# Kernel tuning notes

Measured on AMD Instinct MI355X. Metric: run time of the kernel, lower is better.

The kernel has to match this reference:

```python
import jax, jax.numpy as jnp
import numpy as np

DIM = 1024
NUM_HEADS = 16
HEAD_DIM = DIM // NUM_HEADS
THETA = 10000.0


def apply_rope(x):
    # x: [B, S, H, D]; Llama-style interleaved rotary pairs.
    S, D = x.shape[1], x.shape[3]
    half = D // 2
    inv_freq = THETA ** (-jnp.arange(half, dtype=jnp.float32) * 2.0 / D)  # [D/2]
    angles = jnp.arange(S, dtype=jnp.float32)[:, None] * inv_freq[None, :]  # [S, D/2]
    cos = jnp.cos(angles)[None, :, None, :]  # [1,S,1,D/2]
    sin = jnp.sin(angles)[None, :, None, :]
    x_even = x[..., 0::2]
    x_odd = x[..., 1::2]
    out_even = x_even * cos - x_odd * sin
    out_odd = x_even * sin + x_odd * cos
    out = jnp.stack([out_even, out_odd], axis=-1).reshape(x.shape)
    return out.astype(x.dtype)


def setup_inputs() -> dict:
    key = jax.random.key(0)
    ks = jax.random.split(key, 5)
    B, S = 2, 2048
    x = jax.random.normal(ks[0], (B, S, DIM), dtype=jnp.float32)
    scale = 1.0 / np.sqrt(DIM)
    Wq = jax.random.normal(ks[1], (DIM, DIM), dtype=jnp.float32) * scale
    Wk = jax.random.normal(ks[2], (DIM, DIM), dtype=jnp.float32) * scale
    Wv = jax.random.normal(ks[3], (DIM, DIM), dtype=jnp.float32) * scale
    Wo = jax.random.normal(ks[4], (DIM, DIM), dtype=jnp.float32) * scale
    return {"x": x, "Wq": Wq, "Wk": Wk, "Wv": Wv, "Wo": Wo}


def reference(x, Wq, Wk, Wv, Wo):
    B, S, _ = x.shape
    # torch Linear: y = x @ W^T
    q = (x @ Wq.T).reshape(B, S, NUM_HEADS, HEAD_DIM)
    k = (x @ Wk.T).reshape(B, S, NUM_HEADS, HEAD_DIM)
    v = (x @ Wv.T).reshape(B, S, NUM_HEADS, HEAD_DIM)
    q = apply_rope(q)
    k = apply_rope(k)
    # causal SDPA, scale = 1/sqrt(head_dim)
    scale = 1.0 / np.sqrt(HEAD_DIM).astype(np.float32)
    scores = jnp.einsum("bqhd,bkhd->bhqk", q, k) * scale  # [B,H,S,S]
    causal = jnp.tril(jnp.ones((S, S), dtype=bool))
    scores = jnp.where(causal[None, None], scores, jnp.finfo(scores.dtype).min)
    attn = jax.nn.softmax(scores, axis=-1)
    y = jnp.einsum("bhqk,bkhd->bqhd", attn, v).reshape(B, S, DIM)
    return y @ Wo.T
```

## Files before the change

kernel.cpp:

```cpp
#include <hip/hip_runtime.h>
#include <hip/hip_bf16.h>

typedef __attribute__((ext_vector_type(8))) __bf16 bf16x8;
typedef __attribute__((ext_vector_type(4))) __bf16 bf16x4;
typedef __attribute__((ext_vector_type(4))) float f32x4;
typedef __attribute__((ext_vector_type(16))) float f32x16;
typedef __attribute__((ext_vector_type(2))) unsigned int uint2v;
typedef __attribute__((ext_vector_type(4))) unsigned int uint4v;

#define DIM 1024
#define SLEN 2048
#define NH 16
#define HD 64

__device__ __forceinline__ f32x4 MFMA(bf16x8 a, bf16x8 b, f32x4 c) {
    return __builtin_amdgcn_mfma_f32_16x16x32_bf16(a, b, c, 0, 0, 0);
}
__device__ __forceinline__ f32x16 MFMA32(bf16x8 a, bf16x8 b, f32x16 c) {
    return __builtin_amdgcn_mfma_f32_32x32x16_bf16(a, b, c, 0, 0, 0);
}
__device__ __forceinline__ unsigned cvtpk(float a, float b) {
    unsigned r;
    asm("v_cvt_pk_bf16_f32 %0, %1, %2" : "=v"(r) : "v"(a), "v"(b));
    return r;
}

__global__ __launch_bounds__(256) void cvt_bf16(const float* __restrict__ in,
                                                __bf16* __restrict__ out, int n) {
    int i = (blockIdx.x * blockDim.x + threadIdx.x) * 8;
    if (i >= n) return;
    f32x4 a = *reinterpret_cast<const f32x4*>(in + i);
    f32x4 b = *reinterpret_cast<const f32x4*>(in + i + 4);
    bf16x8 o;
#pragma unroll
    for (int j = 0; j < 4; ++j) { o[j] = (__bf16)a[j]; o[j + 4] = (__bf16)b[j]; }
    *reinterpret_cast<bf16x8*>(out + i) = o;
}

__global__ __launch_bounds__(256) void cvt_w4(const float* __restrict__ w0,
                                              const float* __restrict__ w1,
                                              const float* __restrict__ w2,
                                              const float* __restrict__ w3,
                                              __bf16* __restrict__ o0,
                                              __bf16* __restrict__ o1,
                                              __bf16* __restrict__ o2,
                                              __bf16* __restrict__ o3) {
    int s = blockIdx.y;
    const float* in = s == 0 ? w0 : s == 1 ? w1 : s == 2 ? w2 : w3;
    __bf16* out = s == 0 ? o0 : s == 1 ? o1 : s == 2 ? o2 : o3;
    int i = (blockIdx.x * blockDim.x + threadIdx.x) * 8;
    f32x4 a = *reinterpret_cast<const f32x4*>(in + i);
    f32x4 b = *reinterpret_cast<const f32x4*>(in + i + 4);
    bf16x8 o;
#pragma unroll
    for (int j = 0; j < 4; ++j) { o[j] = (__bf16)a[j]; o[j + 4] = (__bf16)b[j]; }
    *reinterpret_cast<bf16x8*>(out + i) = o;
}

__global__ __launch_bounds__(256) void rope2(__bf16* __restrict__ q,
                                             __bf16* __restrict__ k) {
    __bf16* t = blockIdx.y == 0 ? q : k;
    const float scale = blockIdx.y == 0 ? 0.18033688011112042f : 1.0f;
    int idx = blockIdx.x * blockDim.x + threadIdx.x;
    int row = idx >> 9;
    int p = idx & 511;
    int head = p >> 5;
    int j = p & 31;
    int s = row & (SLEN - 1);
    float inv = expf(-0.28782313662425574f * (float)j);
    float angle = (float)s * inv;
    float sn, cs;
    sincosf(angle, &sn, &cs);
    size_t base = (size_t)row * DIM + head * HD + 2 * j;
    float e = (float)t[base], o = (float)t[base + 1];
    t[base] = (__bf16)((e * cs - o * sn) * scale);
    t[base + 1] = (__bf16)((e * sn + o * cs) * scale);
}

__global__ __launch_bounds__(256) void gemm_qkv(const __bf16* __restrict__ X,
                                                const __bf16* __restrict__ Wq,
                                                const __bf16* __restrict__ Wk,
                                                const __bf16* __restrict__ Wv,
                                                __bf16* __restrict__ Qo,
                                                __bf16* __restrict__ Ko,
                                                __bf16* __restrict__ Vt) {
    __shared__ alignas(16) __bf16 Alds[128 * 64];
    __shared__ alignas(16) __bf16 Blds[128 * 64];
    const int tid = threadIdx.x;
    const int lane = tid & 63;
    const int w = tid >> 6;
    const int wr = w >> 1, wc = w & 1;
    const int l15 = lane & 15, lhi = lane >> 4;
    const int l7 = l15 & 7;
    const int m0 = blockIdx.y * 128;
    const int n0g = blockIdx.x * 128;
    const int seg = n0g >> 10;
    const int n0 = n0g & 1023;
    const __bf16* __restrict__ B = seg == 0 ? Wq : seg == 1 ? Wk : Wv;
    const int K = 1024, N = 1024;

    const int lrow = lane >> 3;
    const int scol = ((lane & 7) ^ lrow) * 8;

    f32x4 acc[4][4] = {};

    for (int kt = 0; kt < K; kt += 64) {
#pragma unroll
        for (int c = 0; c < 4; ++c) {
            int r0 = c * 32 + w * 8;
            const __bf16* sa = &X[(size_t)(m0 + r0 + lrow) * K + kt + scol];
            const __bf16* sb = &B[(size_t)(n0 + r0 + lrow) * K + kt + scol];
            __builtin_amdgcn_global_load_lds((const __attribute__((address_space(1))) void*)sa,
                                             (__attribute__((address_space(3))) void*)&Alds[r0 * 64],
                                             16, 0, 0);
            __builtin_amdgcn_global_load_lds((const __attribute__((address_space(1))) void*)sb,
                                             (__attribute__((address_space(3))) void*)&Blds[r0 * 64],
                                             16, 0, 0);
        }
        __syncthreads();
#pragma unroll
        for (int kk = 0; kk < 2; ++kk) {
            bf16x8 af[4], bfr[4];
#pragma unroll
            for (int i = 0; i < 4; ++i) {
                af[i] = *(const bf16x8*)&Alds[(wr * 64 + i * 16 + l15) * 64 + 8 * ((kk * 4 + lhi) ^ l7)];
                bfr[i] = *(const bf16x8*)&Blds[(wc * 64 + i * 16 + l15) * 64 + 8 * ((kk * 4 + lhi) ^ l7)];
            }
            __builtin_amdgcn_s_setprio(1);
#pragma unroll
            for (int i = 0; i < 4; ++i)
#pragma unroll
                for (int j = 0; j < 4; ++j)
                    acc[i][j] = MFMA(af[i], bfr[j], acc[i][j]);
            __builtin_amdgcn_s_setprio(0);
        }
        __syncthreads();
    }
    if (seg < 2) {
        __bf16* __restrict__ O = seg == 0 ? Qo : Ko;
#pragma unroll
        for (int i = 0; i < 4; ++i)
#pragma unroll
            for (int j = 0; j < 4; ++j)
#pragma unroll
                for (int r = 0; r < 4; ++r) {
                    int row = m0 + wr * 64 + i * 16 + lhi * 4 + r;
                    int col = n0 + wc * 64 + j * 16 + l15;
                    O[(size_t)row * N + col] = (__bf16)acc[i][j][r];
                }
    } else {
#pragma unroll
        for (int i = 0; i < 4; ++i)
#pragma unroll
            for (int j = 0; j < 4; ++j) {
                int row = m0 + wr * 64 + i * 16 + lhi * 4;
                int col = n0 + wc * 64 + j * 16 + l15;
                int bb = row >> 11, s = row & 2047;
                int hh = col >> 6, d = col & 63;
                bf16x4 pk;
#pragma unroll
                for (int r = 0; r < 4; ++r) pk[r] = (__bf16)acc[i][j][r];
                *(bf16x4*)&Vt[((size_t)(bb * 16 + hh) * 64 + d) * SLEN + s] = pk;
            }
    }
}

__global__ __launch_bounds__(256) void gemm_o(const __bf16* __restrict__ A,
                                              const __bf16* __restrict__ B,
                                              float* __restrict__ C) {
    __shared__ alignas(16) __bf16 Alds[64 * 64];
    __shared__ alignas(16) __bf16 Blds[128 * 64];
    const int tid = threadIdx.x;
    const int lane = tid & 63;
    const int w = tid >> 6;
    const int wr = w >> 1, wc = w & 1;
    const int l15 = lane & 15, lhi = lane >> 4;
    const int l7 = l15 & 7;
    const int m0 = blockIdx.y * 64;
    const int n0 = blockIdx.x * 128;
    const int K = 1024, N = 1024;

    const int lrow = lane >> 3;
    const int scol = ((lane & 7) ^ lrow) * 8;

    f32x4 acc[2][4] = {};

    for (int kt = 0; kt < K; kt += 64) {
#pragma unroll
        for (int c = 0; c < 2; ++c) {
            int r0 = c * 32 + w * 8;
            const __bf16* sa = &A[(size_t)(m0 + r0 + lrow) * K + kt + scol];
            __builtin_amdgcn_global_load_lds((const __attribute__((address_space(1))) void*)sa,
                                             (__attribute__((address_space(3))) void*)&Alds[r0 * 64],
                                             16, 0, 0);
        }
#pragma unroll
        for (int c = 0; c < 4; ++c) {
            int r0 = c * 32 + w * 8;
            const __bf16* sb = &B[(size_t)(n0 + r0 + lrow) * K + kt + scol];
            __builtin_amdgcn_global_load_lds((const __attribute__((address_space(1))) void*)sb,
                                             (__attribute__((address_space(3))) void*)&Blds[r0 * 64],
                                             16, 0, 0);
        }
        __syncthreads();
#pragma unroll
        for (int kk = 0; kk < 2; ++kk) {
            bf16x8 af[2], bfr[4];
#pragma unroll
            for (int i = 0; i < 2; ++i)
                af[i] = *(const bf16x8*)&Alds[(wr * 32 + i * 16 + l15) * 64 + 8 * ((kk * 4 + lhi) ^ l7)];
#pragma unroll
            for (int j = 0; j < 4; ++j)
                bfr[j] = *(const bf16x8*)&Blds[(wc * 64 + j * 16 + l15) * 64 + 8 * ((kk * 4 + lhi) ^ l7)];
            __builtin_amdgcn_s_setprio(1);
#pragma unroll
            for (int i = 0; i < 2; ++i)
#pragma unroll
                for (int j = 0; j < 4; ++j)
                    acc[i][j] = MFMA(af[i], bfr[j], acc[i][j]);
            __builtin_amdgcn_s_setprio(0);
        }
        __syncthreads();
    }
#pragma unroll
    for (int i = 0; i < 2; ++i)
#pragma unroll
        for (int j = 0; j < 4; ++j)
#pragma unroll
            for (int r = 0; r < 4; ++r) {
                int row = m0 + wr * 32 + i * 16 + lhi * 4 + r;
                int col = n0 + wc * 64 + j * 16 + l15;
                C[(size_t)row * N + col] = acc[i][j][r];
            }
}

__global__ __launch_bounds__(256, 4) void attn_kernel(const __bf16* __restrict__ Q,
                                                      const __bf16* __restrict__ K,
                                                      const __bf16* __restrict__ Vt,
                                                      __bf16* __restrict__ Y) {
    __shared__ __bf16 Klds[2][64 * 64];
    __shared__ __bf16 Vlds[2][64 * 64];

    const int tid = threadIdx.x;
    const int lane = tid & 63;
    const int w = tid >> 6;
    const int qhalf = w & 1, khalf = w >> 1;
    const int l31 = lane & 31;
    const int hi32 = lane >> 5;
    const int l7 = l31 & 7;

    const int id = blockIdx.x;
    const int x = id & 7, jj = id >> 3;
    const int qi = jj >> 2;
    const int g = qi >> 3, r = qi & 7;
    const int qt = g == 0 ? 31 - r : g == 1 ? r : g == 2 ? 23 - r : 8 + r;
    const int bh = 4 * x + (jj & 3);
    const int b = bh >> 4, h = bh & 15;

    const int srow = lane >> 3;
    const int scs = (lane & 7) ^ srow;
    const __bf16* skP = K + (size_t)b * SLEN * DIM + h * HD + (size_t)(8 * w + srow) * DIM + scs * 8;
    const __bf16* svP = Vt + (size_t)bh * 64 * SLEN + (size_t)(8 * w + srow) * SLEN + scs * 8;
    const int dA = (8 * w + srow) * 64;

    auto stage = [&](int buf) {
#pragma unroll
        for (int i = 0; i < 2; ++i) {
            __builtin_amdgcn_global_load_lds(
                (const __attribute__((address_space(1))) void*)(skP + (size_t)i * 32 * DIM),
                (__attribute__((address_space(3))) void*)&Klds[buf][dA + i * 32 * 64], 16, 0, 0);
            __builtin_amdgcn_global_load_lds(
                (const __attribute__((address_space(1))) void*)(svP + (size_t)i * 32 * SLEN),
                (__attribute__((address_space(3))) void*)&Vlds[buf][dA + i * 32 * 64], 16, 0, 0);
        }
        skP += 64 * DIM;
        svP += 64;
    };

    const int qloc = qhalf * 32 + l31;
    const int qg = qt * 64 + qloc;
    const size_t qbase = (size_t)(b * SLEN + qg) * DIM + h * HD;
    bf16x8 qf0 = *(const bf16x8*)&Q[qbase + 0 + 8 * hi32];
    bf16x8 qf1 = *(const bf16x8*)&Q[qbase + 16 + 8 * hi32];
    bf16x8 qf2 = *(const bf16x8*)&Q[qbase + 32 + 8 * hi32];
    bf16x8 qf3 = *(const bf16x8*)&Q[qbase + 48 + 8 * hi32];

    const int krowbase = (khalf * 32 + l31) * 64;
    const int koff0 = krowbase + 8 * ((0 + hi32) ^ l7);
    const int koff1 = krowbase + 8 * ((2 + hi32) ^ l7);
    const int koff2 = krowbase + 8 * ((4 + hi32) ^ l7);
    const int koff3 = krowbase + 8 * ((6 + hi32) ^ l7);
    const int vrow0 = l31 * 64, vrow1 = (32 + l31) * 64;
    const int voff00 = vrow0 + 8 * ((4 * khalf + 0 + hi32) ^ l7);
    const int voff01 = vrow0 + 8 * ((4 * khalf + 2 + hi32) ^ l7);
    const int voff10 = vrow1 + 8 * ((4 * khalf + 0 + hi32) ^ l7);
    const int voff11 = vrow1 + 8 * ((4 * khalf + 2 + hi32) ^ l7);

    bf16x8 ones;
#pragma unroll
    for (int t = 0; t < 8; ++t) ones[t] = (__bf16)1.0f;

    f32x16 acc0 = {}, acc1 = {};
    f32x16 accL = {};

    const int nkt = qt + 1;
    stage(0);
    for (int kt = 0; kt < nkt; ++kt) {
        const int cur = kt & 1;
        __syncthreads();
        if (kt + 1 < nkt) stage(cur ^ 1);
        const __bf16* Kc = Klds[cur];
        const __bf16* Vc = Vlds[cur];

        f32x16 S = {};
        __builtin_amdgcn_s_setprio(1);
        S = MFMA32(*(const bf16x8*)&Kc[koff0], qf0, S);
        S = MFMA32(*(const bf16x8*)&Kc[koff1], qf1, S);
        S = MFMA32(*(const bf16x8*)&Kc[koff2], qf2, S);
        S = MFMA32(*(const bf16x8*)&Kc[koff3], qf3, S);
        __builtin_amdgcn_s_setprio(0);

        if (kt == qt) {
#pragma unroll
            for (int r2 = 0; r2 < 16; ++r2) {
                const int krow = (r2 & 3) + 8 * (r2 >> 2) + 4 * hi32 + 32 * khalf;
                if (krow > qloc) S[r2] = -1e30f;
            }
        }
        float p[16];
#pragma unroll
        for (int r2 = 0; r2 < 16; ++r2) p[r2] = exp2f(S[r2] - 16.0f);

        bf16x8 pf[2];
#pragma unroll
        for (int ss = 0; ss < 2; ++ss) {
            unsigned P01 = cvtpk(p[8 * ss + 0], p[8 * ss + 1]);
            unsigned P23 = cvtpk(p[8 * ss + 2], p[8 * ss + 3]);
            unsigned Q01 = cvtpk(p[8 * ss + 4], p[8 * ss + 5]);
            unsigned Q23 = cvtpk(p[8 * ss + 6], p[8 * ss + 7]);
            uint2v sa = __builtin_amdgcn_permlane32_swap(P01, Q01, false, false);
            uint2v sb = __builtin_amdgcn_permlane32_swap(P23, Q23, false, false);
            uint4v pwv = {sa[0], sb[0], sa[1], sb[1]};
            pf[ss] = __builtin_bit_cast(bf16x8, pwv);
        }

        __builtin_amdgcn_s_setprio(1);
        accL = MFMA32(ones, pf[0], accL);
        accL = MFMA32(ones, pf[1], accL);
        acc0 = MFMA32(*(const bf16x8*)&Vc[voff00], pf[0], acc0);
        acc0 = MFMA32(*(const bf16x8*)&Vc[voff01], pf[1], acc0);
        acc1 = MFMA32(*(const bf16x8*)&Vc[voff10], pf[0], acc1);
        acc1 = MFMA32(*(const bf16x8*)&Vc[voff11], pf[1], acc1);
        __builtin_amdgcn_s_setprio(0);
    }

    float lsum = accL[0];
    float* fbuf = (float*)&Klds[0][0];
    float* lbuf = (float*)&Vlds[0][0];
    __syncthreads();
    if (khalf == 1) {
#pragma unroll
        for (int r2 = 0; r2 < 16; ++r2) {
            fbuf[(qhalf * 2 + 0) * 1024 + r2 * 64 + lane] = acc0[r2];
            fbuf[(qhalf * 2 + 1) * 1024 + r2 * 64 + lane] = acc1[r2];
        }
        lbuf[qhalf * 64 + lane] = lsum;
    }
    __syncthreads();
    if (khalf == 0) {
#pragma unroll
        for (int r2 = 0; r2 < 16; ++r2) {
            acc0[r2] += fbuf[(qhalf * 2 + 0) * 1024 + r2 * 64 + lane];
            acc1[r2] += fbuf[(qhalf * 2 + 1) * 1024 + r2 * 64 + lane];
        }
        lsum += lbuf[qhalf * 64 + lane];
        const float inv = 1.0f / lsum;
        const size_t obase = (size_t)(b * SLEN + qg) * DIM + h * HD;
#pragma unroll
        for (int gg = 0; gg < 4; ++gg) {
            bf16x4 o0, o1;
#pragma unroll
            for (int e = 0; e < 4; ++e) {
                o0[e] = (__bf16)(acc0[gg * 4 + e] * inv);
                o1[e] = (__bf16)(acc1[gg * 4 + e] * inv);
            }
            *(bf16x4*)&Y[obase + 8 * gg + 4 * hi32] = o0;
            *(bf16x4*)&Y[obase + 32 + 8 * gg + 4 * hi32] = o1;
        }
    }
}

extern "C" void kernel_launch(void* const* d_in, const int* in_sizes, int n_in,
                              void* d_out, int out_size, void* d_ws, size_t ws_size,
                              hipStream_t stream) {
    const float* x = (const float*)d_in[0];
    const float* Wq = (const float*)d_in[1];
    const float* Wk = (const float*)d_in[2];
    const float* Wv = (const float*)d_in[3];
    const float* Wo = (const float*)d_in[4];
    float* out = (float*)d_out;

    const size_t XN = (size_t)4096 * 1024;
    const size_t WN = (size_t)1024 * 1024;

    __bf16* xb = (__bf16*)d_ws;
    __bf16* qb = xb + XN;
    __bf16* kb = qb + XN;
    __bf16* vtb = kb + XN;
    __bf16* wqb = vtb + XN;
    __bf16* wkb = wqb + WN;
    __bf16* wvb = wkb + WN;
    __bf16* wob = wvb + WN;
    __bf16* yb = xb;

    cvt_bf16<<<XN / 8 / 256, 256, 0, stream>>>(x, xb, (int)XN);
    dim3 gw(WN / 8 / 256, 4);
    cvt_w4<<<gw, 256, 0, stream>>>(Wq, Wk, Wv, Wo, wqb, wkb, wvb, wob);

    dim3 gq(24, 32);
    gemm_qkv<<<gq, 256, 0, stream>>>(xb, wqb, wkb, wvb, qb, kb, vtb);

    int pairs = 4096 * (DIM / 2);
    dim3 gr(pairs / 256, 2);
    rope2<<<gr, 256, 0, stream>>>(qb, kb);

    attn_kernel<<<1024, 256, 0, stream>>>(qb, kb, vtb, yb);

    dim3 go(8, 64);
    gemm_o<<<go, 256, 0, stream>>>(yb, wob, out);
}
```

Baseline: 109.3 us.

## Load K/V tiles directly from global into registers, dropping LDS staging

The attention kernel no longer stages K and V tiles into double-buffered shared memory via global_load_lds with per-iteration barriers. Each wave now loads its own K and V fragments straight from global memory into registers inside the loop, and shared memory is kept only for the final cross-wave reduction. This removes the per-tile __syncthreads and LDS traffic, but loses explicit prefetch overlap. Each K/V element is also now fetched by two waves, relying on cache hits.

```diff
diff --git a/kernel.cpp b/kernel.cpp
--- a/kernel.cpp
+++ b/kernel.cpp
@@ -238,8 +238,8 @@
                                                       const __bf16* __restrict__ K,
                                                       const __bf16* __restrict__ Vt,
                                                       __bf16* __restrict__ Y) {
-    __shared__ __bf16 Klds[2][64 * 64];
-    __shared__ __bf16 Vlds[2][64 * 64];
+    __shared__ float fbuf[4096];
+    __shared__ float lbuf[128];
 
     const int tid = threadIdx.x;
     const int lane = tid & 63;
@@ -247,7 +247,6 @@
     const int qhalf = w & 1, khalf = w >> 1;
     const int l31 = lane & 31;
     const int hi32 = lane >> 5;
-    const int l7 = l31 & 7;
 
     const int id = blockIdx.x;
     const int x = id & 7, jj = id >> 3;
@@ -257,25 +256,9 @@
     const int bh = 4 * x + (jj & 3);
     const int b = bh >> 4, h = bh & 15;
 
-    const int srow = lane >> 3;
-    const int scs = (lane & 7) ^ srow;
-    const __bf16* skP = K + (size_t)b * SLEN * DIM + h * HD + (size_t)(8 * w + srow) * DIM + scs * 8;
-    const __bf16* svP = Vt + (size_t)bh * 64 * SLEN + (size_t)(8 * w + srow) * SLEN + scs * 8;
-    const int dA = (8 * w + srow) * 64;
-
-    auto stage = [&](int buf) {
-#pragma unroll
-        for (int i = 0; i < 2; ++i) {
-            __builtin_amdgcn_global_load_lds(
-                (const __attribute__((address_space(1))) void*)(skP + (size_t)i * 32 * DIM),
-                (__attribute__((address_space(3))) void*)&Klds[buf][dA + i * 32 * 64], 16, 0, 0);
-            __builtin_amdgcn_global_load_lds(
-                (const __attribute__((address_space(1))) void*)(svP + (size_t)i * 32 * SLEN),
-                (__attribute__((address_space(3))) void*)&Vlds[buf][dA + i * 32 * 64], 16, 0, 0);
-        }
-        skP += 64 * DIM;
-        svP += 64;
-    };
+    const __bf16* kPtr = K + (size_t)(b * SLEN + khalf * 32 + l31) * DIM + h * HD + 8 * hi32;
+    const __bf16* vPtr0 = Vt + (size_t)(bh * 64 + l31) * SLEN + 32 * khalf + 8 * hi32;
+    const __bf16* vPtr1 = vPtr0 + (size_t)32 * SLEN;
 
     const int qloc = qhalf * 32 + l31;
     const int qg = qt * 64 + qloc;
@@ -285,17 +268,6 @@
     bf16x8 qf2 = *(const bf16x8*)&Q[qbase + 32 + 8 * hi32];
     bf16x8 qf3 = *(const bf16x8*)&Q[qbase + 48 + 8 * hi32];
 
-    const int krowbase = (khalf * 32 + l31) * 64;
-    const int koff0 = krowbase + 8 * ((0 + hi32) ^ l7);
-    const int koff1 = krowbase + 8 * ((2 + hi32) ^ l7);
-    const int koff2 = krowbase + 8 * ((4 + hi32) ^ l7);
-    const int koff3 = krowbase + 8 * ((6 + hi32) ^ l7);
-    const int vrow0 = l31 * 64, vrow1 = (32 + l31) * 64;
-    const int voff00 = vrow0 + 8 * ((4 * khalf + 0 + hi32) ^ l7);
-    const int voff01 = vrow0 + 8 * ((4 * khalf + 2 + hi32) ^ l7);
-    const int voff10 = vrow1 + 8 * ((4 * khalf + 0 + hi32) ^ l7);
-    const int voff11 = vrow1 + 8 * ((4 * khalf + 2 + hi32) ^ l7);
-
     bf16x8 ones;
 #pragma unroll
     for (int t = 0; t < 8; ++t) ones[t] = (__bf16)1.0f;
@@ -304,21 +276,27 @@
     f32x16 accL = {};
 
     const int nkt = qt + 1;
-    stage(0);
     for (int kt = 0; kt < nkt; ++kt) {
-        const int cur = kt & 1;
-        __syncthreads();
-        if (kt + 1 < nkt) stage(cur ^ 1);
-        const __bf16* Kc = Klds[cur];
-        const __bf16* Vc = Vlds[cur];
+        bf16x8 k0 = *(const bf16x8*)(kPtr + 0);
+        bf16x8 k1 = *(const bf16x8*)(kPtr + 16);
+        bf16x8 k2 = *(const bf16x8*)(kPtr + 32);
+        bf16x8 k3 = *(const bf16x8*)(kPtr + 48);
+        kPtr += (size_t)64 * DIM;
 
         f32x16 S = {};
         __builtin_amdgcn_s_setprio(1);
-        S = MFMA32(*(const bf16x8*)&Kc[koff0], qf0, S);
-        S = MFMA32(*(const bf16x8*)&Kc[koff1], qf1, S);
-        S = MFMA32(*(const bf16x8*)&Kc[koff2], qf2, S);
-        S = MFMA32(*(const bf16x8*)&Kc[koff3], qf3, S);
+        S = MFMA32(k0, qf0, S);
+        S = MFMA32(k1, qf1, S);
+        S = MFMA32(k2, qf2, S);
+        S = MFMA32(k3, qf3, S);
         __builtin_amdgcn_s_setprio(0);
+
+        bf16x8 v00 = *(const bf16x8*)(vPtr0 + 0);
+        bf16x8 v01 = *(const bf16x8*)(vPtr0 + 16);
+        bf16x8 v10 = *(const bf16x8*)(vPtr1 + 0);
+        bf16x8 v11 = *(const bf16x8*)(vPtr1 + 16);
+        vPtr0 += 64;
+        vPtr1 += 64;
 
         if (kt == qt) {
 #pragma unroll
@@ -347,17 +325,14 @@
         __builtin_amdgcn_s_setprio(1);
         accL = MFMA32(ones, pf[0], accL);
         accL = MFMA32(ones, pf[1], accL);
-        acc0 = MFMA32(*(const bf16x8*)&Vc[voff00], pf[0], acc0);
-        acc0 = MFMA32(*(const bf16x8*)&Vc[voff01], pf[1], acc0);
-        acc1 = MFMA32(*(const bf16x8*)&Vc[voff10], pf[0], acc1);
-        acc1 = MFMA32(*(const bf16x8*)&Vc[voff11], pf[1], acc1);
+        acc0 = MFMA32(v00, pf[0], acc0);
+        acc0 = MFMA32(v01, pf[1], acc0);
+        acc1 = MFMA32(v10, pf[0], acc1);
+        acc1 = MFMA32(v11, pf[1], acc1);
         __builtin_amdgcn_s_setprio(0);
     }
 
     float lsum = accL[0];
-    float* fbuf = (float*)&Klds[0][0];
-    float* lbuf = (float*)&Vlds[0][0];
-    __syncthreads();
     if (khalf == 1) {
 #pragma unroll
         for (int r2 = 0; r2 < 16; ++r2) {
```

After: 136.0 us. +24.4%, slower.
